# Performance work log

Hardware: AMD Instinct MI355X
Metric: run time of the kernel (lower is better)

Reference implementation:

```python
import jax, jax.numpy as jnp
import numpy as np

N, M, C = 32768, 8192, 128
K = 3            # number of interpolation neighbors (PointNet++/RepSurf FP)
EPS_BN = 1e-5    # torch BatchNorm1d default eps
EPS_D = 1e-8     # RepSurf dist_recip eps


def setup_inputs() -> dict:
    key = jax.random.key(0)
    ks = jax.random.split(key, 16)
    s = 0.05
    inp = {
        "pos1": jax.random.normal(ks[0], (N, 3), jnp.float32),
        "pos2": jax.random.normal(ks[1], (M, 3), jnp.float32),
        "feat2": jax.random.normal(ks[2], (M, C), jnp.float32),
    }
    # MLP stack [128,128,128]: Linear + BatchNorm1d (gamma/beta) per layer
    for i in range(3):
        inp[f"W{i}"] = jax.random.normal(ks[3 + i], (C, C), jnp.float32) * s
        inp[f"b{i}"] = jnp.zeros((C,), jnp.float32)
        inp[f"g{i}"] = jnp.ones((C,), jnp.float32)
        inp[f"be{i}"] = jnp.zeros((C,), jnp.float32)
    return inp


def _lin_bn_relu(x, W, b, g, be):
    # Linear -> BatchNorm1d (training-mode batch stats, biased var) -> ReLU
    y = x @ W.T + b
    m = y.mean(axis=0)
    v = y.var(axis=0)
    return jax.nn.relu((y - m) * jax.lax.rsqrt(v + EPS_BN) * g + be)


def reference(pos1, pos2, feat2, W0, b0, g0, be0, W1, b1, g1, be1, W2, b2, g2, be2):
    # squared pairwise distances [N, M] (memory-bound: 1 GB fp32)
    d = ((pos1 ** 2).sum(-1, keepdims=True)
         + (pos2 ** 2).sum(-1)[None, :]
         - 2.0 * (pos1 @ pos2.T))
    neg_d, idx = jax.lax.top_k(-d, K)          # 3 nearest neighbors
    dk = jnp.maximum(-neg_d, 0.0)              # [N, K] squared dists
    w = 1.0 / (dk + EPS_D)
    w = w / w.sum(-1, keepdims=True)           # inverse-distance weights
    # gather neighbor features and interpolate: [N, K, C] -> [N, C]
    interp = jnp.einsum('nkc,nk->nc', feat2[idx], w)
    x = _lin_bn_relu(interp, W0, b0, g0, be0)
    x = _lin_bn_relu(x, W1, b1, g1, be1)
    x = _lin_bn_relu(x, W2, b2, g2, be2)
    return x
```

## Files before the change

kernel.cpp:

```cpp
#include <hip/hip_runtime.h>
#include <math.h>

#define NQ 32768
#define MC 8192
#define CC 128
#define EPS_BN 1e-5f
#define EPS_D  1e-8

#define DBL_BIG 1e300
#define IDX_BIG 0x7fffffff

#define QB  64
#define TB  512
#define NW  8
#define CH  2048
#define HM  (MC / 2)
#define NCH (HM / CH)
#define SLC (CH / NW)
#define KMASK 0xFFFFE000u
#define IMASK 0x1FFFu
#define NSURV 64
#define KNN_B ((NQ / QB) * 2)
#define GEMM_B (NQ / 64)
#define NGRP 8

typedef __attribute__((ext_vector_type(8))) short bf16x8;
typedef __attribute__((ext_vector_type(4))) float floatx4;
typedef unsigned short ushort_t;

__device__ __forceinline__ unsigned umin_(unsigned a, unsigned b) { return a < b ? a : b; }
__device__ __forceinline__ unsigned umax_(unsigned a, unsigned b) { return a > b ? a : b; }
#define KSWAP(a, b) { unsigned t_ = umin_(a, b); b = umax_(a, b); a = t_; }

__device__ __forceinline__ unsigned bf16pair(float a, float b) {
    unsigned ua = __float_as_uint(a); ua = (ua + 0x7FFFu + ((ua >> 16) & 1u)) >> 16;
    unsigned ub = __float_as_uint(b); ub = (ub + 0x7FFFu + ((ub >> 16) & 1u)) >> 16;
    return ua | (ub << 16);
}
__device__ __forceinline__ ushort_t bf16one(float a) {
    unsigned ua = __float_as_uint(a);
    return (ushort_t)((ua + 0x7FFFu + ((ua >> 16) & 1u)) >> 16);
}
__device__ __forceinline__ float bflo(unsigned u) { return __uint_as_float(u << 16); }
__device__ __forceinline__ float bfhi(unsigned u) { return __uint_as_float(u & 0xFFFF0000u); }

__global__ __launch_bounds__(TB) void knn_kernel(const float* __restrict__ pos1,
                                                 const float* __restrict__ pos2,
                                                 unsigned* __restrict__ skeys,
                                                 const float* __restrict__ W0,
                                                 const float* __restrict__ W1,
                                                 const float* __restrict__ W2,
                                                 ushort_t* __restrict__ Wbf,
                                                 float* __restrict__ stats) {
    __shared__ __align__(16) float4 sp4[CH * 3 / 4];
    __shared__ unsigned skey[QB][NW * 4];

    if (blockIdx.x >= KNN_B) {
        const int pb = blockIdx.x - KNN_B;
        const int f = pb * TB + threadIdx.x;
        const float* Ws[3] = {W0, W1, W2};
#pragma unroll
        for (int l = 0; l < 3; ++l) {
            const float4 v = ((const float4*)Ws[l])[f];
            unsigned* dst = (unsigned*)(Wbf + (size_t)l * CC * CC);
            dst[f * 2 + 0] = bf16pair(v.x, v.y);
            dst[f * 2 + 1] = bf16pair(v.z, v.w);
        }
        if (pb == 0)
            for (int i = threadIdx.x; i < 3 * NGRP * 256; i += TB) stats[i] = 0.f;
        return;
    }

    const int half = blockIdx.x & 1;
    const int bq   = blockIdx.x >> 1;
    const int wv = threadIdx.x >> 6;
    const int ln = threadIdx.x & 63;
    const int q  = bq * QB + ln;

    const float px = pos1[q * 3 + 0];
    const float py = pos1[q * 3 + 1];
    const float pz = pos1[q * 3 + 2];

    unsigned k0 = 0xFFFFFFFFu, k1 = 0xFFFFFFFFu, k2 = 0xFFFFFFFFu, k3 = 0xFFFFFFFFu;

    for (int c0 = 0; c0 < NCH; ++c0) {
        const int cb = half * HM + c0 * CH;
        __syncthreads();
        {
            const float4* g4 = (const float4*)(pos2 + (size_t)cb * 3);
#pragma unroll
            for (int i = threadIdx.x; i < CH * 3 / 4; i += TB) sp4[i] = g4[i];
        }
        __syncthreads();
        const float4* b4 = sp4 + wv * (SLC * 3 / 4);
        const int jb = cb + wv * SLC;
#pragma unroll 4
        for (int gi = 0; gi < SLC / 4; ++gi) {
            const float4 A = b4[gi * 3 + 0];
            const float4 B = b4[gi * 3 + 1];
            const float4 Cv = b4[gi * 3 + 2];
            const int j = jb + gi * 4;
            const float cx[4] = {A.x, A.w, B.z, Cv.y};
            const float cy[4] = {A.y, B.x, B.w, Cv.z};
            const float cz[4] = {A.z, B.y, Cv.x, Cv.w};
            unsigned e0, e1, e2, e3;
            {
                float dx = px - cx[0], dy = py - cy[0], dz = pz - cz[0];
                e0 = (__float_as_uint(fmaf(dx, dx, fmaf(dy, dy, dz * dz))) & KMASK) | (unsigned)(j + 0);
                dx = px - cx[1]; dy = py - cy[1]; dz = pz - cz[1];
                e1 = (__float_as_uint(fmaf(dx, dx, fmaf(dy, dy, dz * dz))) & KMASK) | (unsigned)(j + 1);
                dx = px - cx[2]; dy = py - cy[2]; dz = pz - cz[2];
                e2 = (__float_as_uint(fmaf(dx, dx, fmaf(dy, dy, dz * dz))) & KMASK) | (unsigned)(j + 2);
                dx = px - cx[3]; dy = py - cy[3]; dz = pz - cz[3];
                e3 = (__float_as_uint(fmaf(dx, dx, fmaf(dy, dy, dz * dz))) & KMASK) | (unsigned)(j + 3);
            }
            KSWAP(e0, e1); KSWAP(e2, e3); KSWAP(e0, e2); KSWAP(e1, e3); KSWAP(e1, e2);
            unsigned m0 = umin_(k0, e3), m1 = umin_(k1, e2);
            unsigned m2 = umin_(k2, e1), m3 = umin_(k3, e0);
            KSWAP(m0, m2); KSWAP(m1, m3); KSWAP(m0, m1); KSWAP(m2, m3);
            k0 = m0; k1 = m1; k2 = m2; k3 = m3;
        }
    }
    skey[ln][wv * 4 + 0] = k0;
    skey[ln][wv * 4 + 1] = k1;
    skey[ln][wv * 4 + 2] = k2;
    skey[ln][wv * 4 + 3] = k3;
    __syncthreads();

#pragma unroll
    for (int t = threadIdx.x * 4; t < threadIdx.x * 4 + 4; ++t) {
        const int ql = t >> 5, slot = t & 31;
        skeys[(size_t)(bq * QB + ql) * NSURV + half * 32 + slot] = skey[ql][slot];
    }
}

template <int MODE>
__global__ __launch_bounds__(256) void gemm_mfma(const void* __restrict__ Xsrc_,
                                                 const unsigned* __restrict__ skeys,
                                                 const float* __restrict__ pos1,
                                                 const float* __restrict__ pos2,
                                                 const float* __restrict__ statsIn,
                                                 const float* __restrict__ gIn,
                                                 const float* __restrict__ beIn,
                                                 const ushort_t* __restrict__ Wb,
                                                 const float* __restrict__ bias,
                                                 ushort_t* __restrict__ Y,
                                                 float* __restrict__ statsOut) {
    __shared__ __align__(16) short xa[64][136];
    __shared__ __align__(16) short wb[128][136];
    __shared__ float blk_s[CC], blk_q[CC];
    __shared__ float sc_l[CC], sh_l[CC];

    const int row0 = blockIdx.x * 64;

    if constexpr (MODE == 0) {
        const float* feat2 = (const float*)Xsrc_;
        __shared__ int   lidx[QB][3];
        __shared__ float lw[QB][3];
        {
            double* rrd = (double*)&xa[0][0];
            int*    rri = (int*)&wb[0][0];
            const int ql = threadIdx.x >> 2;
            const int pp = threadIdx.x & 3;
            const int qg = row0 + ql;
            const double qx = (double)pos1[qg * 3 + 0];
            const double qy = (double)pos1[qg * 3 + 1];
            const double qz = (double)pos1[qg * 3 + 2];
            double b0 = DBL_BIG, b1 = DBL_BIG, b2 = DBL_BIG;
            int    j0 = IDX_BIG, j1 = IDX_BIG, j2 = IDX_BIG;
            const uint4* kp = (const uint4*)(skeys + (size_t)qg * NSURV + pp * 16);
#pragma unroll
            for (int gi = 0; gi < 4; ++gi) {
                const uint4 kk = kp[gi];
                const unsigned ks[4] = {kk.x, kk.y, kk.z, kk.w};
#pragma unroll
                for (int u = 0; u < 4; ++u) {
                    const int id = (int)(ks[u] & IMASK);
                    const double x = (double)pos2[id * 3 + 0];
                    const double y = (double)pos2[id * 3 + 1];
                    const double z = (double)pos2[id * 3 + 2];
                    const double ax = qx - x, ay = qy - y, az = qz - z;
                    const double d = ax * ax + ay * ay + az * az;
                    const bool l2 = (d < b2) || (d == b2 && id < j2);
                    if (l2) {
                        const bool l1 = (d < b1) || (d == b1 && id < j1);
                        const bool l0 = (d < b0) || (d == b0 && id < j0);
                        b2 = l1 ? b1 : d;              j2 = l1 ? j1 : id;
                        b1 = l1 ? (l0 ? b0 : d) : b1;  j1 = l1 ? (l0 ? j0 : id) : j1;
                        b0 = l0 ? d : b0;              j0 = l0 ? id : j0;
                    }
                }
            }
            const int base = (ql * 4 + pp) * 3;
            rrd[base + 0] = b0; rri[base + 0] = j0;
            rrd[base + 1] = b1; rri[base + 1] = j1;
            rrd[base + 2] = b2; rri[base + 2] = j2;
            __syncthreads();
            if (threadIdx.x < QB) {
                const int qq = threadIdx.x;
                double c0 = DBL_BIG, c1 = DBL_BIG, c2 = DBL_BIG;
                int    i0 = IDX_BIG, i1 = IDX_BIG, i2 = IDX_BIG;
#pragma unroll
                for (int s = 0; s < 12; ++s) {
                    const double d = rrd[qq * 12 + s];
                    const int   id = rri[qq * 12 + s];
                    const bool l2 = (d < c2) || (d == c2 && id < i2);
                    if (l2) {
                        const bool l1 = (d < c1) || (d == c1 && id < i1);
                        const bool l0 = (d < c0) || (d == c0 && id < i0);
                        c2 = l1 ? c1 : d;              i2 = l1 ? i1 : id;
                        c1 = l1 ? (l0 ? c0 : d) : c1;  i1 = l1 ? (l0 ? i0 : id) : i1;
                        c0 = l0 ? d : c0;              i0 = l0 ? id : i0;
                    }
                }
                const double r0 = 1.0 / (c0 + EPS_D);
                const double r1 = 1.0 / (c1 + EPS_D);
                const double r2 = 1.0 / (c2 + EPS_D);
                const double inv = 1.0 / (r0 + r1 + r2);
                lidx[qq][0] = i0; lidx[qq][1] = i1; lidx[qq][2] = i2;
                lw[qq][0] = (float)(r0 * inv);
                lw[qq][1] = (float)(r1 * inv);
                lw[qq][2] = (float)(r2 * inv);
            }
            __syncthreads();
        }
        if (threadIdx.x < CC) { blk_s[threadIdx.x] = 0.f; blk_q[threadIdx.x] = 0.f; }
#pragma unroll
        for (int e = threadIdx.x; e < 64 * 32; e += 256) {
            const int r = e >> 5, c4 = e & 31;
            const int i0 = lidx[r][0], i1 = lidx[r][1], i2 = lidx[r][2];
            const float w0 = lw[r][0], w1 = lw[r][1], w2 = lw[r][2];
            const float4 f0 = *(const float4*)&feat2[(size_t)i0 * CC + c4 * 4];
            const float4 f1 = *(const float4*)&feat2[(size_t)i1 * CC + c4 * 4];
            const float4 f2 = *(const float4*)&feat2[(size_t)i2 * CC + c4 * 4];
            float4 v;
            v.x = w0 * f0.x + w1 * f1.x + w2 * f2.x;
            v.y = w0 * f0.y + w1 * f1.y + w2 * f2.y;
            v.z = w0 * f0.z + w1 * f1.z + w2 * f2.z;
            v.w = w0 * f0.w + w1 * f1.w + w2 * f2.w;
            unsigned* dst = (unsigned*)&xa[r][0];
            dst[c4 * 2 + 0] = bf16pair(v.x, v.y);
            dst[c4 * 2 + 1] = bf16pair(v.z, v.w);
        }
    } else {
        const ushort_t* Xbf = (const ushort_t*)Xsrc_;
        if (threadIdx.x < CC) {
            const int c = threadIdx.x;
            float s = 0.f, q = 0.f;
#pragma unroll
            for (int gr = 0; gr < NGRP; ++gr) {
                s += statsIn[gr * 256 + c];
                q += statsIn[gr * 256 + CC + c];
            }
            const float m = s * (1.f / (float)NQ);
            const float v = fmaf(-m, m, q * (1.f / (float)NQ));
            const float rstd = rsqrtf(v + EPS_BN);
            const float scl = gIn[c] * rstd;
            sc_l[c] = scl;
            sh_l[c] = fmaf(-m, scl, beIn[c]);
            blk_s[c] = 0.f; blk_q[c] = 0.f;
        }
        __syncthreads();
#pragma unroll
        for (int e = threadIdx.x; e < 64 * 16; e += 256) {
            const int r = e >> 4, c8 = e & 15;
            const uint4 u = *(const uint4*)&Xbf[(size_t)(row0 + r) * CC + c8 * 8];
            const float4 s0 = *(const float4*)&sc_l[c8 * 8];
            const float4 s1 = *(const float4*)&sc_l[c8 * 8 + 4];
            const float4 h0 = *(const float4*)&sh_l[c8 * 8];
            const float4 h1 = *(const float4*)&sh_l[c8 * 8 + 4];
            const float v0 = fmaxf(fmaf(bflo(u.x), s0.x, h0.x), 0.f);
            const float v1 = fmaxf(fmaf(bfhi(u.x), s0.y, h0.y), 0.f);
            const float v2 = fmaxf(fmaf(bflo(u.y), s0.z, h0.z), 0.f);
            const float v3 = fmaxf(fmaf(bfhi(u.y), s0.w, h0.w), 0.f);
            const float v4 = fmaxf(fmaf(bflo(u.z), s1.x, h1.x), 0.f);
            const float v5 = fmaxf(fmaf(bfhi(u.z), s1.y, h1.y), 0.f);
            const float v6 = fmaxf(fmaf(bflo(u.w), s1.z, h1.z), 0.f);
            const float v7 = fmaxf(fmaf(bfhi(u.w), s1.w, h1.w), 0.f);
            uint4 o;
            o.x = bf16pair(v0, v1); o.y = bf16pair(v2, v3);
            o.z = bf16pair(v4, v5); o.w = bf16pair(v6, v7);
            *(uint4*)&xa[r][c8 * 8] = o;
        }
    }
#pragma unroll
    for (int e = threadIdx.x; e < 128 * 16; e += 256) {
        const int co = e >> 4, seg = e & 15;
        *(float4*)&wb[co][seg * 8] = *(const float4*)&Wb[(size_t)co * CC + seg * 8];
    }
    __syncthreads();

    const int lane = threadIdx.x & 63;
    const int wv = threadIdx.x >> 6;
    const int nn = lane & 15;
    const int quad = lane >> 4;

    floatx4 acc[8] = {};

    const short* arow = &xa[wv * 16 + nn][0];
#pragma unroll
    for (int ks = 0; ks < 4; ++ks) {
        const bf16x8 a = *(const bf16x8*)(arow + ks * 32 + quad * 8);
#pragma unroll
        for (int ct = 0; ct < 8; ++ct) {
            const bf16x8 b = *(const bf16x8*)(&wb[ct * 16 + nn][0] + ks * 32 + quad * 8);
            acc[ct] = __builtin_amdgcn_mfma_f32_16x16x32_bf16(a, b, acc[ct], 0, 0, 0);
        }
    }

#pragma unroll
    for (int ct = 0; ct < 8; ++ct) {
        const float bv = bias[ct * 16 + nn];
        float s = 0.f, qv = 0.f;
#pragma unroll
        for (int r = 0; r < 4; ++r) {
            acc[ct][r] += bv;
            s += acc[ct][r];
            qv = fmaf(acc[ct][r], acc[ct][r], qv);
        }
#pragma unroll
        for (int r = 0; r < 4; ++r)
            Y[(size_t)(row0 + wv * 16 + quad * 4 + r) * CC + ct * 16 + nn] = bf16one(acc[ct][r]);
        s += __shfl_xor(s, 16, 64); s += __shfl_xor(s, 32, 64);
        qv += __shfl_xor(qv, 16, 64); qv += __shfl_xor(qv, 32, 64);
        if (quad == 0) {
            atomicAdd(&blk_s[ct * 16 + nn], s);
            atomicAdd(&blk_q[ct * 16 + nn], qv);
        }
    }
    __syncthreads();
    {
        const int ch = threadIdx.x;
        const float v = (ch < CC) ? blk_s[ch] : blk_q[ch - CC];
        atomicAdd(&statsOut[(blockIdx.x & (NGRP - 1)) * 256 + ch], v);
    }
}

__global__ __launch_bounds__(256) void bn_final(const ushort_t* __restrict__ Y,
                                                const float* __restrict__ statsIn,
                                                const float* __restrict__ g,
                                                const float* __restrict__ be,
                                                float* __restrict__ out) {
    __shared__ float sc_l[CC], sh_l[CC];
    if (threadIdx.x < CC) {
        const int c = threadIdx.x;
        float s = 0.f, q = 0.f;
#pragma unroll
        for (int gr = 0; gr < NGRP; ++gr) {
            s += statsIn[gr * 256 + c];
            q += statsIn[gr * 256 + CC + c];
        }
        const float m = s * (1.f / (float)NQ);
        const float v = fmaf(-m, m, q * (1.f / (float)NQ));
        const float rstd = rsqrtf(v + EPS_BN);
        const float scl = g[c] * rstd;
        sc_l[c] = scl;
        sh_l[c] = fmaf(-m, scl, be[c]);
    }
    __syncthreads();
    const int base = blockIdx.x * 1024 + threadIdx.x;
#pragma unroll
    for (int it = 0; it < 4; ++it) {
        const int i8 = base + it * 256;
        const int c8 = (i8 & 15) * 8;
        const uint4 u = *(const uint4*)&Y[(size_t)i8 * 8];
        const float4 s0 = *(const float4*)&sc_l[c8];
        const float4 s1 = *(const float4*)&sc_l[c8 + 4];
        const float4 h0 = *(const float4*)&sh_l[c8];
        const float4 h1 = *(const float4*)&sh_l[c8 + 4];
        float4 o0, o1;
        o0.x = fmaxf(fmaf(bflo(u.x), s0.x, h0.x), 0.f);
        o0.y = fmaxf(fmaf(bfhi(u.x), s0.y, h0.y), 0.f);
        o0.z = fmaxf(fmaf(bflo(u.y), s0.z, h0.z), 0.f);
        o0.w = fmaxf(fmaf(bfhi(u.y), s0.w, h0.w), 0.f);
        o1.x = fmaxf(fmaf(bflo(u.z), s1.x, h1.x), 0.f);
        o1.y = fmaxf(fmaf(bfhi(u.z), s1.y, h1.y), 0.f);
        o1.z = fmaxf(fmaf(bflo(u.w), s1.z, h1.z), 0.f);
        o1.w = fmaxf(fmaf(bfhi(u.w), s1.w, h1.w), 0.f);
        ((float4*)out)[i8 * 2 + 0] = o0;
        ((float4*)out)[i8 * 2 + 1] = o1;
    }
}

extern "C" void kernel_launch(void* const* d_in, const int* in_sizes, int n_in,
                              void* d_out, int out_size, void* d_ws, size_t ws_size,
                              hipStream_t stream) {
    (void)in_sizes; (void)n_in; (void)out_size; (void)ws_size;

    const float* pos1  = (const float*)d_in[0];
    const float* pos2  = (const float*)d_in[1];
    const float* feat2 = (const float*)d_in[2];
    const float* Wl[3]  = {(const float*)d_in[3], (const float*)d_in[7],  (const float*)d_in[11]};
    const float* bl[3]  = {(const float*)d_in[4], (const float*)d_in[8],  (const float*)d_in[12]};
    const float* gl[3]  = {(const float*)d_in[5], (const float*)d_in[9],  (const float*)d_in[13]};
    const float* bel[3] = {(const float*)d_in[6], (const float*)d_in[10], (const float*)d_in[14]};

    float* ws = (float*)d_ws;
    ushort_t* B0 = (ushort_t*)ws;
    ushort_t* B1 = B0 + (size_t)NQ * CC;
    unsigned* skeys = (unsigned*)(B1 + (size_t)NQ * CC);
    float* stats = (float*)(skeys + (size_t)NQ * NSURV);
    ushort_t* Wbf = (ushort_t*)(stats + 3 * NGRP * 256);

    float* st0 = stats + 0 * NGRP * 256;
    float* st1 = stats + 1 * NGRP * 256;
    float* st2 = stats + 2 * NGRP * 256;

    knn_kernel<<<KNN_B + 8, TB, 0, stream>>>(pos1, pos2, skeys,
                                             Wl[0], Wl[1], Wl[2], Wbf, stats);
    gemm_mfma<0><<<GEMM_B, 256, 0, stream>>>(feat2, skeys, pos1, pos2,
                                             nullptr, nullptr, nullptr,
                                             Wbf + 0 * CC * CC, bl[0], B0, st0);
    gemm_mfma<1><<<GEMM_B, 256, 0, stream>>>(B0, nullptr, nullptr, nullptr,
                                             st0, gl[0], bel[0],
                                             Wbf + 1 * CC * CC, bl[1], B1, st1);
    gemm_mfma<1><<<GEMM_B, 256, 0, stream>>>(B1, nullptr, nullptr, nullptr,
                                             st1, gl[1], bel[1],
                                             Wbf + 2 * CC * CC, bl[2], B0, st2);
    bn_final<<<GEMM_B, 256, 0, stream>>>(B0, st2, gl[2], bel[2], (float*)d_out);
}
```

Baseline: 203.8 us.

## Rework KNN scan: two queries per thread, expanded distance, med3 top-4 insertion

Each thread in the KNN kernel now handles two query points instead of one, so every candidate read from LDS serves two queries. Candidates are stored in LDS as separate x, y, z arrays plus a precomputed half squared norm. The key becomes half the squared distance, computed as a 3-FMA dot product with the index packed into the low mantissa bits. The sorting-network merge is replaced by a per-candidate fmin plus three fmed3 insertions into a sorted top-4. The aim is fewer VALU instructions and less LDS traffic per candidate pair. The cost is higher register pressure, and the expanded-norm form can round slightly differently or go slightly negative near zero, which relies on later exact reranking of survivors.

```diff
diff --git a/kernel.cpp b/kernel.cpp
--- a/kernel.cpp
+++ b/kernel.cpp
@@ -11,6 +11,7 @@
 #define IDX_BIG 0x7fffffff
 
 #define QB  64
+#define QKB 128
 #define TB  512
 #define NW  8
 #define CH  2048
@@ -20,17 +21,13 @@
 #define KMASK 0xFFFFE000u
 #define IMASK 0x1FFFu
 #define NSURV 64
-#define KNN_B ((NQ / QB) * 2)
+#define KNN_B ((NQ / QKB) * 2)
 #define GEMM_B (NQ / 64)
 #define NGRP 8
 
 typedef __attribute__((ext_vector_type(8))) short bf16x8;
 typedef __attribute__((ext_vector_type(4))) float floatx4;
 typedef unsigned short ushort_t;
-
-__device__ __forceinline__ unsigned umin_(unsigned a, unsigned b) { return a < b ? a : b; }
-__device__ __forceinline__ unsigned umax_(unsigned a, unsigned b) { return a > b ? a : b; }
-#define KSWAP(a, b) { unsigned t_ = umin_(a, b); b = umax_(a, b); a = t_; }
 
 __device__ __forceinline__ unsigned bf16pair(float a, float b) {
     unsigned ua = __float_as_uint(a); ua = (ua + 0x7FFFu + ((ua >> 16) & 1u)) >> 16;
@@ -43,6 +40,24 @@
 }
 __device__ __forceinline__ float bflo(unsigned u) { return __uint_as_float(u << 16); }
 __device__ __forceinline__ float bfhi(unsigned u) { return __uint_as_float(u & 0xFFFF0000u); }
+
+__device__ __forceinline__ void ins4(float& k0, float& k1, float& k2, float& k3, float x) {
+    const float n0 = fminf(k0, x);
+    const float n1 = __builtin_amdgcn_fmed3f(k0, k1, x);
+    const float n2 = __builtin_amdgcn_fmed3f(k1, k2, x);
+    const float n3 = __builtin_amdgcn_fmed3f(k2, k3, x);
+    k0 = n0; k1 = n1; k2 = n2; k3 = n3;
+}
+
+__device__ __forceinline__ float mkkey(float nx, float ny, float nz, float hp,
+                                       float cx, float cy, float cz, float hc,
+                                       unsigned j) {
+    float t = fmaf(nx, cx, hc);
+    t = fmaf(ny, cy, t);
+    t = fmaf(nz, cz, t);
+    t += hp;
+    return __uint_as_float((__float_as_uint(t) & KMASK) | j);
+}
 
 __global__ __launch_bounds__(TB) void knn_kernel(const float* __restrict__ pos1,
                                                  const float* __restrict__ pos2,
@@ -52,8 +67,7 @@
                                                  const float* __restrict__ W2,
                                                  ushort_t* __restrict__ Wbf,
                                                  float* __restrict__ stats) {
-    __shared__ __align__(16) float4 sp4[CH * 3 / 4];
-    __shared__ unsigned skey[QB][NW * 4];
+    __shared__ __align__(16) float sst[4][CH];
 
     if (blockIdx.x >= KNN_B) {
         const int pb = blockIdx.x - KNN_B;
@@ -75,62 +89,68 @@
     const int bq   = blockIdx.x >> 1;
     const int wv = threadIdx.x >> 6;
     const int ln = threadIdx.x & 63;
-    const int q  = bq * QB + ln;
-
-    const float px = pos1[q * 3 + 0];
-    const float py = pos1[q * 3 + 1];
-    const float pz = pos1[q * 3 + 2];
-
-    unsigned k0 = 0xFFFFFFFFu, k1 = 0xFFFFFFFFu, k2 = 0xFFFFFFFFu, k3 = 0xFFFFFFFFu;
+    const int qa = bq * QKB + ln;
+    const int qb = qa + 64;
+
+    const float pax = pos1[qa * 3 + 0], pay = pos1[qa * 3 + 1], paz = pos1[qa * 3 + 2];
+    const float pbx = pos1[qb * 3 + 0], pby = pos1[qb * 3 + 1], pbz = pos1[qb * 3 + 2];
+    const float nxa = -pax, nya = -pay, nza = -paz;
+    const float nxb = -pbx, nyb = -pby, nzb = -pbz;
+    const float hpa = 0.5f * fmaf(pax, pax, fmaf(pay, pay, paz * paz));
+    const float hpb = 0.5f * fmaf(pbx, pbx, fmaf(pby, pby, pbz * pbz));
+
+    const float KINIT = __uint_as_float(0x7F000000u);
+    float a0 = KINIT, a1 = KINIT, a2 = KINIT, a3 = KINIT;
+    float b0 = KINIT, b1 = KINIT, b2 = KINIT, b3 = KINIT;
 
     for (int c0 = 0; c0 < NCH; ++c0) {
         const int cb = half * HM + c0 * CH;
         __syncthreads();
-        {
-            const float4* g4 = (const float4*)(pos2 + (size_t)cb * 3);
-#pragma unroll
-            for (int i = threadIdx.x; i < CH * 3 / 4; i += TB) sp4[i] = g4[i];
+        for (int c = threadIdx.x; c < CH; c += TB) {
+            const float* pp = pos2 + (size_t)(cb + c) * 3;
+            const float x = pp[0], y = pp[1], z = pp[2];
+            sst[0][c] = x; sst[1][c] = y; sst[2][c] = z;
+            sst[3][c] = 0.5f * fmaf(x, x, fmaf(y, y, z * z));
         }
         __syncthreads();
-        const float4* b4 = sp4 + wv * (SLC * 3 / 4);
+        const float4* Xp = (const float4*)&sst[0][wv * SLC];
+        const float4* Yp = (const float4*)&sst[1][wv * SLC];
+        const float4* Zp = (const float4*)&sst[2][wv * SLC];
+        const float4* Hp = (const float4*)&sst[3][wv * SLC];
         const int jb = cb + wv * SLC;
 #pragma unroll 4
         for (int gi = 0; gi < SLC / 4; ++gi) {
-            const float4 A = b4[gi * 3 + 0];
-            const float4 B = b4[gi * 3 + 1];
-            const float4 Cv = b4[gi * 3 + 2];
-            const int j = jb + gi * 4;
-            const float cx[4] = {A.x, A.w, B.z, Cv.y};
-            const float cy[4] = {A.y, B.x, B.w, Cv.z};
-            const float cz[4] = {A.z, B.y, Cv.x, Cv.w};
-            unsigned e0, e1, e2, e3;
-            {
-                float dx = px - cx[0], dy = py - cy[0], dz = pz - cz[0];
-                e0 = (__float_as_uint(fmaf(dx, dx, fmaf(dy, dy, dz * dz))) & KMASK) | (unsigned)(j + 0);
-                dx = px - cx[1]; dy = py - cy[1]; dz = pz - cz[1];
-                e1 = (__float_as_uint(fmaf(dx, dx, fmaf(dy, dy, dz * dz))) & KMASK) | (unsigned)(j + 1);
-                dx = px - cx[2]; dy = py - cy[2]; dz = pz - cz[2];
-                e2 = (__float_as_uint(fmaf(dx, dx, fmaf(dy, dy, dz * dz))) & KMASK) | (unsigned)(j + 2);
-                dx = px - cx[3]; dy = py - cy[3]; dz = pz - cz[3];
-                e3 = (__float_as_uint(fmaf(dx, dx, fmaf(dy, dy, dz * dz))) & KMASK) | (unsigned)(j + 3);
-            }
-            KSWAP(e0, e1); KSWAP(e2, e3); KSWAP(e0, e2); KSWAP(e1, e3); KSWAP(e1, e2);
-            unsigned m0 = umin_(k0, e3), m1 = umin_(k1, e2);
-            unsigned m2 = umin_(k2, e1), m3 = umin_(k3, e0);
-            KSWAP(m0, m2); KSWAP(m1, m3); KSWAP(m0, m1); KSWAP(m2, m3);
-            k0 = m0; k1 = m1; k2 = m2; k3 = m3;
-        }
-    }
-    skey[ln][wv * 4 + 0] = k0;
-    skey[ln][wv * 4 + 1] = k1;
-    skey[ln][wv * 4 + 2] = k2;
-    skey[ln][wv * 4 + 3] = k3;
+            const float4 X = Xp[gi];
+            const float4 Y = Yp[gi];
+            const float4 Z = Zp[gi];
+            const float4 H = Hp[gi];
+            const unsigned j0 = (unsigned)(jb + gi * 4);
+            ins4(a0, a1, a2, a3, mkkey(nxa, nya, nza, hpa, X.x, Y.x, Z.x, H.x, j0 + 0));
+            ins4(a0, a1, a2, a3, mkkey(nxa, nya, nza, hpa, X.y, Y.y, Z.y, H.y, j0 + 1));
+            ins4(a0, a1, a2, a3, mkkey(nxa, nya, nza, hpa, X.z, Y.z, Z.z, H.z, j0 + 2));
+            ins4(a0, a1, a2, a3, mkkey(nxa, nya, nza, hpa, X.w, Y.w, Z.w, H.w, j0 + 3));
+            ins4(b0, b1, b2, b3, mkkey(nxb, nyb, nzb, hpb, X.x, Y.x, Z.x, H.x, j0 + 0));
+            ins4(b0, b1, b2, b3, mkkey(nxb, nyb, nzb, hpb, X.y, Y.y, Z.y, H.y, j0 + 1));
+            ins4(b0, b1, b2, b3, mkkey(nxb, nyb, nzb, hpb, X.z, Y.z, Z.z, H.z, j0 + 2));
+            ins4(b0, b1, b2, b3, mkkey(nxb, nyb, nzb, hpb, X.w, Y.w, Z.w, H.w, j0 + 3));
+        }
+    }
     __syncthreads();
-
-#pragma unroll
-    for (int t = threadIdx.x * 4; t < threadIdx.x * 4 + 4; ++t) {
+    unsigned (*skl)[33] = (unsigned (*)[33])&sst[0][0];
+    skl[ln     ][wv * 4 + 0] = __float_as_uint(a0);
+    skl[ln     ][wv * 4 + 1] = __float_as_uint(a1);
+    skl[ln     ][wv * 4 + 2] = __float_as_uint(a2);
+    skl[ln     ][wv * 4 + 3] = __float_as_uint(a3);
+    skl[ln + 64][wv * 4 + 0] = __float_as_uint(b0);
+    skl[ln + 64][wv * 4 + 1] = __float_as_uint(b1);
+    skl[ln + 64][wv * 4 + 2] = __float_as_uint(b2);
+    skl[ln + 64][wv * 4 + 3] = __float_as_uint(b3);
+    __syncthreads();
+
+#pragma unroll
+    for (int t = threadIdx.x; t < QKB * 32; t += TB) {
         const int ql = t >> 5, slot = t & 31;
-        skeys[(size_t)(bq * QB + ql) * NSURV + half * 32 + slot] = skey[ql][slot];
+        skeys[(size_t)(bq * QKB + ql) * NSURV + half * 32 + slot] = skl[ql][slot];
     }
 }
 
```

Result: slower. 208.7 us (+2.4%).

## Rewrite KNN inner loop with expanded-distance keys and med3 insertion

Applied to the files above, without the earlier changes.

Adds a pack kernel that stores pos2 as float4 with half squared norm, so each candidate's key becomes 0.5|c|^2 - p·c + 0.5|p|^2 computed with three FMAs. The sorting-network top-4 update is replaced by a per-candidate insertion using fmin/fmed3 on float-reinterpreted packed keys. Shared-memory staging and block syncs are removed; each wave reads its slice of candidates directly from global memory with a wave-uniform base. This cuts ALU work per candidate but relies on cached global loads, and the expanded distance form can lose precision and may produce negative values, which changes how the masked keys order.

```diff
diff --git a/kernel.cpp b/kernel.cpp
--- a/kernel.cpp
+++ b/kernel.cpp
@@ -13,10 +13,8 @@
 #define QB  64
 #define TB  512
 #define NW  8
-#define CH  2048
 #define HM  (MC / 2)
-#define NCH (HM / CH)
-#define SLC (CH / NW)
+#define SLCW (HM / NW)
 #define KMASK 0xFFFFE000u
 #define IMASK 0x1FFFu
 #define NSURV 64
@@ -28,10 +26,6 @@
 typedef __attribute__((ext_vector_type(4))) float floatx4;
 typedef unsigned short ushort_t;
 
-__device__ __forceinline__ unsigned umin_(unsigned a, unsigned b) { return a < b ? a : b; }
-__device__ __forceinline__ unsigned umax_(unsigned a, unsigned b) { return a > b ? a : b; }
-#define KSWAP(a, b) { unsigned t_ = umin_(a, b); b = umax_(a, b); a = t_; }
-
 __device__ __forceinline__ unsigned bf16pair(float a, float b) {
     unsigned ua = __float_as_uint(a); ua = (ua + 0x7FFFu + ((ua >> 16) & 1u)) >> 16;
     unsigned ub = __float_as_uint(b); ub = (ub + 0x7FFFu + ((ub >> 16) & 1u)) >> 16;
@@ -44,16 +38,47 @@
 __device__ __forceinline__ float bflo(unsigned u) { return __uint_as_float(u << 16); }
 __device__ __forceinline__ float bfhi(unsigned u) { return __uint_as_float(u & 0xFFFF0000u); }
 
+__device__ __forceinline__ void ins4(float& k0, float& k1, float& k2, float& k3, float x) {
+    const float n0 = fminf(k0, x);
+    const float n1 = __builtin_amdgcn_fmed3f(k0, k1, x);
+    const float n2 = __builtin_amdgcn_fmed3f(k1, k2, x);
+    const float n3 = __builtin_amdgcn_fmed3f(k2, k3, x);
+    k0 = n0; k1 = n1; k2 = n2; k3 = n3;
+}
+
+__device__ __forceinline__ float mkk(float nx, float ny, float nz, float hp,
+                                     float4 c, unsigned j) {
+    float t = c.w + hp;
+    t = fmaf(nz, c.z, t);
+    t = fmaf(ny, c.y, t);
+    t = fmaf(nx, c.x, t);
+    return __uint_as_float((__float_as_uint(t) & KMASK) | j);
+}
+
+__global__ __launch_bounds__(TB) void pack_kernel(const float* __restrict__ pos2,
+                                                  float4* __restrict__ pos2pk) {
+    const int c0 = blockIdx.x * (MC / 8);
+#pragma unroll
+    for (int c = c0 + threadIdx.x; c < c0 + MC / 8; c += TB) {
+        const float x = pos2[c * 3 + 0];
+        const float y = pos2[c * 3 + 1];
+        const float z = pos2[c * 3 + 2];
+        float4 v;
+        v.x = x; v.y = y; v.z = z;
+        v.w = 0.5f * fmaf(x, x, fmaf(y, y, z * z));
+        pos2pk[c] = v;
+    }
+}
+
 __global__ __launch_bounds__(TB) void knn_kernel(const float* __restrict__ pos1,
-                                                 const float* __restrict__ pos2,
+                                                 const float4* __restrict__ pos2pk,
                                                  unsigned* __restrict__ skeys,
                                                  const float* __restrict__ W0,
                                                  const float* __restrict__ W1,
                                                  const float* __restrict__ W2,
                                                  ushort_t* __restrict__ Wbf,
                                                  float* __restrict__ stats) {
-    __shared__ __align__(16) float4 sp4[CH * 3 / 4];
-    __shared__ unsigned skey[QB][NW * 4];
+    __shared__ unsigned skl[QB][33];
 
     if (blockIdx.x >= KNN_B) {
         const int pb = blockIdx.x - KNN_B;
@@ -73,64 +98,45 @@
 
     const int half = blockIdx.x & 1;
     const int bq   = blockIdx.x >> 1;
-    const int wv = threadIdx.x >> 6;
     const int ln = threadIdx.x & 63;
+    const int wvu = __builtin_amdgcn_readfirstlane((int)(threadIdx.x >> 6));
     const int q  = bq * QB + ln;
 
     const float px = pos1[q * 3 + 0];
     const float py = pos1[q * 3 + 1];
     const float pz = pos1[q * 3 + 2];
-
-    unsigned k0 = 0xFFFFFFFFu, k1 = 0xFFFFFFFFu, k2 = 0xFFFFFFFFu, k3 = 0xFFFFFFFFu;
-
-    for (int c0 = 0; c0 < NCH; ++c0) {
-        const int cb = half * HM + c0 * CH;
-        __syncthreads();
-        {
-            const float4* g4 = (const float4*)(pos2 + (size_t)cb * 3);
-#pragma unroll
-            for (int i = threadIdx.x; i < CH * 3 / 4; i += TB) sp4[i] = g4[i];
-        }
-        __syncthreads();
-        const float4* b4 = sp4 + wv * (SLC * 3 / 4);
-        const int jb = cb + wv * SLC;
+    const float nx = -px, ny = -py, nz = -pz;
+    const float hp = 0.5f * fmaf(px, px, fmaf(py, py, pz * pz));
+
+    const int jb = half * HM + wvu * SLCW;
+    const float4* cp = pos2pk + jb;
+
+    const float KINIT = __uint_as_float(0x7F000000u);
+    float k0 = KINIT, k1 = KINIT, k2 = KINIT, k3 = KINIT;
+
 #pragma unroll 4
-        for (int gi = 0; gi < SLC / 4; ++gi) {
-            const float4 A = b4[gi * 3 + 0];
-            const float4 B = b4[gi * 3 + 1];
-            const float4 Cv = b4[gi * 3 + 2];
-            const int j = jb + gi * 4;
-            const float cx[4] = {A.x, A.w, B.z, Cv.y};
-            const float cy[4] = {A.y, B.x, B.w, Cv.z};
-            const float cz[4] = {A.z, B.y, Cv.x, Cv.w};
-            unsigned e0, e1, e2, e3;
-            {
-                float dx = px - cx[0], dy = py - cy[0], dz = pz - cz[0];
-                e0 = (__float_as_uint(fmaf(dx, dx, fmaf(dy, dy, dz * dz))) & KMASK) | (unsigned)(j + 0);
-                dx = px - cx[1]; dy = py - cy[1]; dz = pz - cz[1];
-                e1 = (__float_as_uint(fmaf(dx, dx, fmaf(dy, dy, dz * dz))) & KMASK) | (unsigned)(j + 1);
-                dx = px - cx[2]; dy = py - cy[2]; dz = pz - cz[2];
-                e2 = (__float_as_uint(fmaf(dx, dx, fmaf(dy, dy, dz * dz))) & KMASK) | (unsigned)(j + 2);
-                dx = px - cx[3]; dy = py - cy[3]; dz = pz - cz[3];
-                e3 = (__float_as_uint(fmaf(dx, dx, fmaf(dy, dy, dz * dz))) & KMASK) | (unsigned)(j + 3);
-            }
-            KSWAP(e0, e1); KSWAP(e2, e3); KSWAP(e0, e2); KSWAP(e1, e3); KSWAP(e1, e2);
-            unsigned m0 = umin_(k0, e3), m1 = umin_(k1, e2);
-            unsigned m2 = umin_(k2, e1), m3 = umin_(k3, e0);
-            KSWAP(m0, m2); KSWAP(m1, m3); KSWAP(m0, m1); KSWAP(m2, m3);
-            k0 = m0; k1 = m1; k2 = m2; k3 = m3;
-        }
-    }
-    skey[ln][wv * 4 + 0] = k0;
-    skey[ln][wv * 4 + 1] = k1;
-    skey[ln][wv * 4 + 2] = k2;
-    skey[ln][wv * 4 + 3] = k3;
+    for (int gi = 0; gi < SLCW / 4; ++gi) {
+        const float4 c0 = cp[gi * 4 + 0];
+        const float4 c1 = cp[gi * 4 + 1];
+        const float4 c2 = cp[gi * 4 + 2];
+        const float4 c3 = cp[gi * 4 + 3];
+        const unsigned j0 = (unsigned)(jb + gi * 4);
+        ins4(k0, k1, k2, k3, mkk(nx, ny, nz, hp, c0, j0 + 0));
+        ins4(k0, k1, k2, k3, mkk(nx, ny, nz, hp, c1, j0 + 1));
+        ins4(k0, k1, k2, k3, mkk(nx, ny, nz, hp, c2, j0 + 2));
+        ins4(k0, k1, k2, k3, mkk(nx, ny, nz, hp, c3, j0 + 3));
+    }
+
+    skl[ln][wvu * 4 + 0] = __float_as_uint(k0);
+    skl[ln][wvu * 4 + 1] = __float_as_uint(k1);
+    skl[ln][wvu * 4 + 2] = __float_as_uint(k2);
+    skl[ln][wvu * 4 + 3] = __float_as_uint(k3);
     __syncthreads();
 
 #pragma unroll
     for (int t = threadIdx.x * 4; t < threadIdx.x * 4 + 4; ++t) {
         const int ql = t >> 5, slot = t & 31;
-        skeys[(size_t)(bq * QB + ql) * NSURV + half * 32 + slot] = skey[ql][slot];
+        skeys[(size_t)(bq * QB + ql) * NSURV + half * 32 + slot] = skl[ql][slot];
     }
 }
 
@@ -401,12 +407,14 @@
     unsigned* skeys = (unsigned*)(B1 + (size_t)NQ * CC);
     float* stats = (float*)(skeys + (size_t)NQ * NSURV);
     ushort_t* Wbf = (ushort_t*)(stats + 3 * NGRP * 256);
+    float4* pos2pk = (float4*)(Wbf + 3 * CC * CC);
 
     float* st0 = stats + 0 * NGRP * 256;
     float* st1 = stats + 1 * NGRP * 256;
     float* st2 = stats + 2 * NGRP * 256;
 
-    knn_kernel<<<KNN_B + 8, TB, 0, stream>>>(pos1, pos2, skeys,
+    pack_kernel<<<8, TB, 0, stream>>>(pos2, pos2pk);
+    knn_kernel<<<KNN_B + 8, TB, 0, stream>>>(pos1, pos2pk, skeys,
                                              Wl[0], Wl[1], Wl[2], Wbf, stats);
     gemm_mfma<0><<<GEMM_B, 256, 0, stream>>>(feat2, skeys, pos1, pos2,
                                              nullptr, nullptr, nullptr,
```

After: 211.7 us. +3.9%, slower.
